# Optimization experiments

Hardware: AMD Instinct MI355X
Metric: run time of the kernel (lower is better)

The kernel has to match this reference:

```python
import jax, jax.numpy as jnp
import numpy as np

D_DIM = 100000  # vocabulary size
W_DIM = 128     # embedding width
BATCH = 4096    # number of (center, context) index pairs


def setup_inputs() -> dict:
    key = jax.random.key(0)
    k1, k2, kw1, kb1, kw2, kb2 = jax.random.split(key, 6)
    idx1 = jax.random.randint(k1, (BATCH,), 0, D_DIM, dtype=jnp.int64 if jax.config.jax_enable_x64 else jnp.int32)
    idx2 = jax.random.randint(k2, (BATCH,), 0, D_DIM, dtype=jnp.int64 if jax.config.jax_enable_x64 else jnp.int32)
    # torch.nn.Linear(D, W): weight [W, D], bias [W], uniform(-1/sqrt(D), 1/sqrt(D))
    bound = 1.0 / np.sqrt(D_DIM)
    W1 = jax.random.uniform(kw1, (W_DIM, D_DIM), jnp.float32, -bound, bound)
    b1 = jax.random.uniform(kb1, (W_DIM,), jnp.float32, -bound, bound)
    W2 = jax.random.uniform(kw2, (W_DIM, D_DIM), jnp.float32, -bound, bound)
    b2 = jax.random.uniform(kb2, (W_DIM,), jnp.float32, -bound, bound)
    return {"idx1": idx1, "idx2": idx2, "W1": W1, "b1": b1, "W2": W2, "b2": b2}


def reference(idx1, idx2, W1, b1, W2, b2):
    # Linear(one_hot(idx)) == weight[:, idx] + bias  -> direct row (column) gather.
    p1 = W1[:, idx1].T + b1              # [B, W_dim]
    p2 = W2[:, idx2].T + b2              # [B, W_dim]
    s = jax.nn.sigmoid(jnp.sum(p1 * p2, axis=-1))  # [B]
    # original: cat([1 - sigmoid, sigmoid]) -> [B, 2]
    return jnp.stack([1.0 - s, s], axis=-1)
```

## Files before the change

kernel.cpp:

```cpp
#include <hip/hip_runtime.h>
#include <math.h>

#define D_DIM 100000
#define W_DIM 128
#define BATCH 4096
#define NBUCK 6250
#define BPAD  7168

__global__ __launch_bounds__(1024) void bucket_sort(
    const int* __restrict__ idx1, const int* __restrict__ idx2,
    unsigned int* __restrict__ packed)
{
    __shared__ int cnt[BPAD];
    __shared__ int ranks[BATCH];
    __shared__ int psum[1024];

    const int m = blockIdx.x;
    const int* __restrict__ idx = m ? idx2 : idx1;
    const int t = threadIdx.x;

    for (int i = t; i < BPAD; i += 1024) cnt[i] = 0;
    __syncthreads();

    for (int i = t; i < BATCH; i += 1024)
        ranks[i] = atomicAdd(&cnt[idx[i] >> 4], 1);
    __syncthreads();

    const int base = t * 7;
    int s = 0;
    #pragma unroll
    for (int j = 0; j < 7; ++j) s += cnt[base + j];
    psum[t] = s;
    __syncthreads();

    for (int off = 1; off < 1024; off <<= 1) {
        int v = (t >= off) ? psum[t - off] : 0;
        __syncthreads();
        psum[t] += v;
        __syncthreads();
    }

    int run = (t == 0) ? 0 : psum[t - 1];
    #pragma unroll
    for (int j = 0; j < 7; ++j) {
        int c = cnt[base + j];
        cnt[base + j] = run;
        run += c;
    }
    __syncthreads();

    for (int i = t; i < BATCH; i += 1024) {
        const int v = idx[i];
        const int pos = cnt[v >> 4] + ranks[i];
        packed[m * BATCH + pos] = ((unsigned)v << 12) | (unsigned)i;
    }
}

__global__ __launch_bounds__(256) void gather(
    const unsigned int* __restrict__ packed,
    const float* __restrict__ W1, const float* __restrict__ b1,
    const float* __restrict__ W2, const float* __restrict__ b2,
    float* __restrict__ P)
{
    const int bid   = blockIdx.x;
    const int m     = bid >> 10;
    const int local = bid & 1023;
    const int nb = ((local & 7) << 7) | (local >> 3);
    const int p  = (nb << 2) + (threadIdx.x >> 6);
    const int l  = threadIdx.x & 63;

    const unsigned int pk = packed[(m << 12) + p];
    const int b = pk & 4095;
    const int i = (int)(pk >> 12);

    const float* __restrict__ W  = m ? W2 : W1;
    const float* __restrict__ bb = m ? b2 : b1;

    const float v0 = W[(size_t)l * D_DIM + i] + bb[l];
    const float v1 = W[(size_t)(l + 64) * D_DIM + i] + bb[l + 64];

    float* dst = P + (((size_t)(m << 12) + b) << 7);
    dst[l]      = v0;
    dst[l + 64] = v1;
}

__global__ __launch_bounds__(256) void dot_sig(
    const float* __restrict__ P, float* __restrict__ out)
{
    const int b = (blockIdx.x << 2) + (threadIdx.x >> 6);
    const int l = threadIdx.x & 63;

    const float2 x = ((const float2*)(P + ((size_t)b << 7)))[l];
    const float2 y = ((const float2*)(P + ((size_t)(BATCH + b) << 7)))[l];
    float v = x.x * y.x + x.y * y.y;

    #pragma unroll
    for (int off = 32; off > 0; off >>= 1)
        v += __shfl_down(v, off, 64);

    if (l == 0) {
        const float s = 1.0f / (1.0f + expf(-v));
        ((float2*)out)[b] = make_float2(1.0f - s, s);
    }
}

extern "C" void kernel_launch(void* const* d_in, const int* in_sizes, int n_in,
                              void* d_out, int out_size, void* d_ws, size_t ws_size,
                              hipStream_t stream)
{
    const int*   idx1 = (const int*)  d_in[0];
    const int*   idx2 = (const int*)  d_in[1];
    const float* W1   = (const float*)d_in[2];
    const float* b1   = (const float*)d_in[3];
    const float* W2   = (const float*)d_in[4];
    const float* b2   = (const float*)d_in[5];
    float* out = (float*)d_out;

    unsigned int* packed = (unsigned int*)d_ws;
    float* P = (float*)((char*)d_ws + 32768);

    bucket_sort<<<2, 1024, 0, stream>>>(idx1, idx2, packed);
    gather<<<2048, 256, 0, stream>>>(packed, W1, b1, W2, b2, P);
    dot_sig<<<BATCH / 4, 256, 0, stream>>>(P, out);
}
```

Before: 133.5 us.

## Use wave-shuffle scan in bucket sort and gather two entries per wave

The bucket-sort prefix sum now uses a two-level wavefront shuffle scan instead of a 1024-step shared-memory Hillis-Steele scan with many barriers. The gather kernel has each wave handle two packed entries instead of one, which halves the block count, and it remaps blocks so that each XCD gets a contiguous chunk of sorted entries. The aim is to cut barrier and synchronisation cost in the sort and to raise memory-level parallelism and locality in the gather, at the cost of fewer blocks in flight.

```diff
diff --git a/kernel.cpp b/kernel.cpp
--- a/kernel.cpp
+++ b/kernel.cpp
@@ -4,7 +4,6 @@
 #define D_DIM 100000
 #define W_DIM 128
 #define BATCH 4096
-#define NBUCK 6250
 #define BPAD  7168
 
 __global__ __launch_bounds__(1024) void bucket_sort(
@@ -13,46 +12,61 @@
 {
     __shared__ int cnt[BPAD];
     __shared__ int ranks[BATCH];
-    __shared__ int psum[1024];
+    __shared__ int wsum[16];
 
     const int m = blockIdx.x;
     const int* __restrict__ idx = m ? idx2 : idx1;
-    const int t = threadIdx.x;
+    const int t    = threadIdx.x;
+    const int lane = t & 63;
+    const int wv   = t >> 6;
 
     for (int i = t; i < BPAD; i += 1024) cnt[i] = 0;
     __syncthreads();
 
-    for (int i = t; i < BATCH; i += 1024)
+    #pragma unroll
+    for (int j = 0; j < 4; ++j) {
+        const int i = t + j * 1024;
         ranks[i] = atomicAdd(&cnt[idx[i] >> 4], 1);
+    }
     __syncthreads();
 
     const int base = t * 7;
-    int s = 0;
+    int c[7]; int s = 0;
     #pragma unroll
-    for (int j = 0; j < 7; ++j) s += cnt[base + j];
-    psum[t] = s;
+    for (int j = 0; j < 7; ++j) { c[j] = cnt[base + j]; s += c[j]; }
+
+    int inc = s;
+    #pragma unroll
+    for (int off = 1; off < 64; off <<= 1) {
+        const int v = __shfl_up(inc, off, 64);
+        if (lane >= off) inc += v;
+    }
+    if (lane == 63) wsum[wv] = inc;
     __syncthreads();
 
-    for (int off = 1; off < 1024; off <<= 1) {
-        int v = (t >= off) ? psum[t - off] : 0;
-        __syncthreads();
-        psum[t] += v;
-        __syncthreads();
-    }
-
-    int run = (t == 0) ? 0 : psum[t - 1];
-    #pragma unroll
-    for (int j = 0; j < 7; ++j) {
-        int c = cnt[base + j];
-        cnt[base + j] = run;
-        run += c;
+    if (t < 16) {
+        const int v = wsum[t];
+        int winc = v;
+        #pragma unroll
+        for (int off = 1; off < 16; off <<= 1) {
+            const int u = __shfl_up(winc, off, 16);
+            if (t >= off) winc += u;
+        }
+        wsum[t] = winc - v;
     }
     __syncthreads();
 
-    for (int i = t; i < BATCH; i += 1024) {
+    int excl = wsum[wv] + (inc - s);
+    #pragma unroll
+    for (int j = 0; j < 7; ++j) { cnt[base + j] = excl; excl += c[j]; }
+    __syncthreads();
+
+    #pragma unroll
+    for (int j = 0; j < 4; ++j) {
+        const int i = t + j * 1024;
         const int v = idx[i];
-        const int pos = cnt[v >> 4] + ranks[i];
-        packed[m * BATCH + pos] = ((unsigned)v << 12) | (unsigned)i;
+        packed[(m << 12) + cnt[v >> 4] + ranks[i]] =
+            ((unsigned)v << 12) | (unsigned)i;
     }
 }
 
@@ -62,26 +76,39 @@
     const float* __restrict__ W2, const float* __restrict__ b2,
     float* __restrict__ P)
 {
-    const int bid   = blockIdx.x;
-    const int m     = bid >> 10;
-    const int local = bid & 1023;
-    const int nb = ((local & 7) << 7) | (local >> 3);
-    const int p  = (nb << 2) + (threadIdx.x >> 6);
-    const int l  = threadIdx.x & 63;
+    const int bid = blockIdx.x;
+    const int xcd = bid & 7;
+    const int seq = bid >> 3;
+    const int wv  = threadIdx.x >> 6;
+    const int l   = threadIdx.x & 63;
 
-    const unsigned int pk = packed[(m << 12) + p];
-    const int b = pk & 4095;
-    const int i = (int)(pk >> 12);
+    const int e0 = (xcd << 10) + (seq << 3) + (wv << 1);
+    const int m  = e0 >> 12;
 
     const float* __restrict__ W  = m ? W2 : W1;
     const float* __restrict__ bb = m ? b2 : b1;
 
-    const float v0 = W[(size_t)l * D_DIM + i] + bb[l];
-    const float v1 = W[(size_t)(l + 64) * D_DIM + i] + bb[l + 64];
+    const unsigned pk0 = packed[e0];
+    const unsigned pk1 = packed[e0 + 1];
+    const int b0 = pk0 & 4095; const int i0 = (int)(pk0 >> 12);
+    const int b1v = pk1 & 4095; const int i1 = (int)(pk1 >> 12);
 
-    float* dst = P + (((size_t)(m << 12) + b) << 7);
-    dst[l]      = v0;
-    dst[l + 64] = v1;
+    const float* colA = W + (size_t)l * D_DIM;
+    const float* colB = W + (size_t)(l + 64) * D_DIM;
+    const float a0 = colA[i0];
+    const float a1 = colA[i1];
+    const float a2 = colB[i0];
+    const float a3 = colB[i1];
+
+    const float biasA = bb[l];
+    const float biasB = bb[l + 64];
+
+    float* dst0 = P + (((size_t)(m << 12) + b0)  << 7);
+    float* dst1 = P + (((size_t)(m << 12) + b1v) << 7);
+    dst0[l]      = a0 + biasA;
+    dst0[l + 64] = a2 + biasB;
+    dst1[l]      = a1 + biasA;
+    dst1[l + 64] = a3 + biasB;
 }
 
 __global__ __launch_bounds__(256) void dot_sig(
@@ -120,6 +147,6 @@
     float* P = (float*)((char*)d_ws + 32768);
 
     bucket_sort<<<2, 1024, 0, stream>>>(idx1, idx2, packed);
-    gather<<<2048, 256, 0, stream>>>(packed, W1, b1, W2, b2, P);
+    gather<<<1024, 256, 0, stream>>>(packed, W1, b1, W2, b2, P);
     dot_sig<<<BATCH / 4, 256, 0, stream>>>(P, out);
 }
```

Result: no change. 131.7 us (-1.4%).
